# Optimization experiments

Hardware: AMD Instinct MI355X
Metric: run time of the kernel (lower is better)

Reference implementation:

```python
import jax, jax.numpy as jnp
import numpy as np

B, T, C, H, F = 4, 1024, 1024, 16, 4096
D = C // H

def _ln(x, g, b):
    m = x.mean(-1, keepdims=True)
    v = ((x - m) ** 2).mean(-1, keepdims=True)
    return (x - m) * jax.lax.rsqrt(v + 1e-5) * g + b

def setup_inputs() -> dict:
    key = jax.random.key(0)
    ks = jax.random.split(key, 9)
    p = lambda k, shape: jax.random.normal(k, shape, jnp.float32) * 0.02
    return dict(
        x=jax.random.normal(ks[0], (B, T, C), jnp.float32),
        context=jax.random.normal(ks[1], (B, T, C), jnp.float32),
        ln1_g=jnp.ones((C,), jnp.float32), ln1_b=jnp.zeros((C,), jnp.float32),
        qkv_w=p(ks[2], (C, 3 * C)), qkv_b=jnp.zeros((3 * C,), jnp.float32),
        attn_out_w=p(ks[3], (C, C)), attn_out_b=jnp.zeros((C,), jnp.float32),
        lnc_g=jnp.ones((C,), jnp.float32), lnc_b=jnp.zeros((C,), jnp.float32),
        q_w=p(ks[4], (C, C)), q_b=jnp.zeros((C,), jnp.float32),
        kv_w=p(ks[5], (C, 2 * C)), kv_b=jnp.zeros((2 * C,), jnp.float32),
        cross_out_w=p(ks[6], (C, C)), cross_out_b=jnp.zeros((C,), jnp.float32),
        ln2_g=jnp.ones((C,), jnp.float32), ln2_b=jnp.zeros((C,), jnp.float32),
        ffn_w1=p(ks[7], (C, F)), ffn_b1=jnp.zeros((F,), jnp.float32),
        ffn_w2=p(ks[8], (F, C)), ffn_b2=jnp.zeros((C,), jnp.float32),
    )

def reference(x, context, ln1_g, ln1_b, qkv_w, qkv_b, attn_out_w, attn_out_b,
              lnc_g, lnc_b, q_w, q_b, kv_w, kv_b, cross_out_w, cross_out_b,
              ln2_g, ln2_b, ffn_w1, ffn_b1, ffn_w2, ffn_b2):
    scale = 1.0 / np.sqrt(D)
    # --- causal self-attention ---
    h = _ln(x, ln1_g, ln1_b)
    qkv = (h @ qkv_w + qkv_b).reshape(B, T, 3, H, D)
    q, k, v = qkv[:, :, 0], qkv[:, :, 1], qkv[:, :, 2]  # [B,T,H,D]
    s = jnp.einsum('bqhd,bkhd->bhqk', q, k) * scale     # [B,H,T,T]
    causal = jnp.tril(jnp.ones((T, T), bool))
    s = jnp.where(causal, s, -jnp.inf)
    a = jax.nn.softmax(s, axis=-1)
    o = jnp.einsum('bhqk,bkhd->bqhd', a, v).reshape(B, T, C)
    x = x + o @ attn_out_w + attn_out_b
    # --- cross-attention (query=x, context=encoder) ---
    h = _ln(x, lnc_g, lnc_b)
    q = (h @ q_w + q_b).reshape(B, T, H, D)
    kv = (context @ kv_w + kv_b).reshape(B, T, 2, H, D)
    k, v = kv[:, :, 0], kv[:, :, 1]
    s = jnp.einsum('bqhd,bkhd->bhqk', q, k) * scale
    a = jax.nn.softmax(s, axis=-1)
    o = jnp.einsum('bhqk,bkhd->bqhd', a, v).reshape(B, T, C)
    x = x + o @ cross_out_w + cross_out_b
    # --- FFN (exact GELU as in torch default) ---
    h = _ln(x, ln2_g, ln2_b)
    h = jax.nn.gelu(h @ ffn_w1 + ffn_b1, approximate=False)
    return x + h @ ffn_w2 + ffn_b2
```

## Files before the change

### kernel.cpp

```cpp
#include <hip/hip_runtime.h>
#include <hip/hip_bf16.h>

#define BT 4096
#define TT 1024
#define HN 16

typedef __attribute__((ext_vector_type(8))) short bf16x8;
typedef __attribute__((ext_vector_type(4))) float f32x4;

__device__ __forceinline__ unsigned short f2bf(float f) {
    unsigned u = __builtin_bit_cast(unsigned, f);
    unsigned r = (u + 0x7fffu + ((u >> 16) & 1u)) >> 16;
    return (unsigned short)r;
}

__device__ __forceinline__ unsigned pk2bf(float a, float b) {
    return (unsigned)f2bf(a) | ((unsigned)f2bf(b) << 16);
}

__device__ __forceinline__ void g2l16(const void* g, void* l) {
    __builtin_amdgcn_global_load_lds(
        (__attribute__((address_space(1))) void*)(g),
        (__attribute__((address_space(3))) void*)(l), 16, 0, 0);
}

__device__ __forceinline__ float gelu_f(float v) {
    float t = v * (0.7978845608f + 0.0356774081f * v * v);
    float e = __expf(2.f * t);
    float th = 1.f - 2.f / (e + 1.f);
    return 0.5f * v * (1.f + th);
}

struct TransJobs {
    const float* W[7];
    unsigned short* Wt[7];
    int K[7], N[7];
    int start[8];
};

__global__ __launch_bounds__(256)
void transpose_all(TransJobs J)
{
    __shared__ float tile[32][33];
    int bx = blockIdx.x;
    int j = 0;
#pragma unroll
    for (int t = 0; t < 7; ++t)
        if (bx >= J.start[t + 1]) j = t + 1;
    int t = bx - J.start[j];
    int K = J.K[j], N = J.N[j];
    int ntx = N >> 5;
    int n0 = (t % ntx) * 32, k0 = (t / ntx) * 32;
    const float* W = J.W[j];
    unsigned short* Wt = J.Wt[j];
    int tx = threadIdx.x, ty = threadIdx.y;
#pragma unroll
    for (int i = ty; i < 32; i += 8)
        tile[i][tx] = W[(size_t)(k0 + i) * N + n0 + tx];
    __syncthreads();
#pragma unroll
    for (int i = ty; i < 32; i += 8)
        Wt[(size_t)(n0 + i) * K + k0 + tx] = f2bf(tile[tx][i]);
}

__global__ __launch_bounds__(256)
void transpose_v(const unsigned short* __restrict__ v, unsigned short* __restrict__ vt,
                 int stride)
{
    __shared__ unsigned short tile[32][33];
    int d0 = blockIdx.x * 32, t0 = blockIdx.y * 32, bh = blockIdx.z;
    int b = bh >> 4, h = bh & 15;
    int tx = threadIdx.x, ty = threadIdx.y;
#pragma unroll
    for (int i = ty; i < 32; i += 8)
        tile[i][tx] = v[((size_t)b * TT + t0 + i) * stride + h * 64 + d0 + tx];
    __syncthreads();
#pragma unroll
    for (int i = ty; i < 32; i += 8)
        vt[((size_t)bh * 64 + d0 + i) * TT + t0 + tx] = tile[tx][i];
}

__device__ __forceinline__
void ln_row(const float* __restrict__ xr, const float* __restrict__ g,
            const float* __restrict__ bta, unsigned short* __restrict__ outr,
            float* red)
{
    float4 v = ((const float4*)xr)[threadIdx.x];
    float s = v.x + v.y + v.z + v.w;
    float q = v.x*v.x + v.y*v.y + v.z*v.z + v.w*v.w;
#pragma unroll
    for (int m = 1; m < 64; m <<= 1) {
        s += __shfl_xor(s, m, 64);
        q += __shfl_xor(q, m, 64);
    }
    int wave = threadIdx.x >> 6;
    if ((threadIdx.x & 63) == 0) { red[wave] = s; red[4 + wave] = q; }
    __syncthreads();
    s = red[0] + red[1] + red[2] + red[3];
    q = red[4] + red[5] + red[6] + red[7];
    float mean = s * (1.f / 1024.f);
    float var  = q * (1.f / 1024.f) - mean * mean;
    float rstd = rsqrtf(var + 1e-5f);
    float4 gv = ((const float4*)g)[threadIdx.x];
    float4 bv = ((const float4*)bta)[threadIdx.x];
    uint2 o;
    o.x = pk2bf((v.x - mean) * rstd * gv.x + bv.x, (v.y - mean) * rstd * gv.y + bv.y);
    o.y = pk2bf((v.z - mean) * rstd * gv.z + bv.z, (v.w - mean) * rstd * gv.w + bv.w);
    ((uint2*)outr)[threadIdx.x] = o;
}

__global__ __launch_bounds__(256)
void ln_kernel(const float* __restrict__ x, const float* __restrict__ g,
               const float* __restrict__ bta, unsigned short* __restrict__ out)
{
    __shared__ float red[8];
    int row = blockIdx.x;
    ln_row(x + (size_t)row * 1024, g, bta, out + (size_t)row * 1024, red);
}

__global__ __launch_bounds__(256)
void ln_cast(const float* __restrict__ x, const float* __restrict__ g,
             const float* __restrict__ bta, unsigned short* __restrict__ outx,
             const float* __restrict__ ctx, unsigned short* __restrict__ outc)
{
    __shared__ float red[8];
    int bid = blockIdx.x;
    if (bid < BT) {
        ln_row(x + (size_t)bid * 1024, g, bta, outx + (size_t)bid * 1024, red);
    } else {
        size_t i = (size_t)(bid - BT) * 256 + threadIdx.x;
        float4 v = ((const float4*)ctx)[i];
        uint2 o;
        o.x = pk2bf(v.x, v.y);
        o.y = pk2bf(v.z, v.w);
        ((uint2*)outc)[i] = o;
    }
}

template<int MODE>
__device__ __forceinline__
void gemm_core(unsigned short* lA, unsigned short* lB,
               const unsigned short* __restrict__ A,
               const unsigned short* __restrict__ Bt,
               const float* __restrict__ bias,
               const float* __restrict__ res,
               void* __restrict__ outp,
               int N, int K, int m0, int n0, int kbeg, int kend)
{
    const int tid = threadIdx.x;
    const int wave = tid >> 6, lane = tid & 63;
    const int quad = lane >> 4, l16 = lane & 15;
    const int sw = l16 & 7;
    const int wN = (wave >> 1) * 64;
    const int wM = (wave & 1) * 64;

    f32x4 acc[4][4];
#pragma unroll
    for (int i = 0; i < 4; ++i)
#pragma unroll
        for (int j = 0; j < 4; ++j)
#pragma unroll
            for (int r = 0; r < 4; ++r) acc[i][j][r] = 0.f;

    for (int k0 = kbeg; k0 < kend; k0 += 64) {
        __syncthreads();
#pragma unroll
        for (int it = 0; it < 4; ++it) {
            int chunk = it * 256 + tid;
            int row = chunk >> 3, slot = chunk & 7;
            int kc = slot ^ (row & 7);
            g2l16(A  + (size_t)(m0 + row) * K + k0 + kc * 8, &lA[chunk * 8]);
            g2l16(Bt + (size_t)(n0 + row) * K + k0 + kc * 8, &lB[chunk * 8]);
        }
        __syncthreads();
#pragma unroll
        for (int kk = 0; kk < 64; kk += 32) {
            const int gc = (kk >> 3) + quad;
            const int sl = (gc ^ sw) * 8;
            bf16x8 af[4], bfr[4];
#pragma unroll
            for (int i = 0; i < 4; ++i)
                af[i] = *(const bf16x8*)&lB[(wN + i * 16 + l16) * 64 + sl];
#pragma unroll
            for (int j = 0; j < 4; ++j)
                bfr[j] = *(const bf16x8*)&lA[(wM + j * 16 + l16) * 64 + sl];
#pragma unroll
            for (int i = 0; i < 4; ++i)
#pragma unroll
                for (int j = 0; j < 4; ++j)
                    acc[i][j] = __builtin_amdgcn_mfma_f32_16x16x32_bf16(af[i], bfr[j], acc[i][j], 0, 0, 0);
        }
    }

#pragma unroll
    for (int i = 0; i < 4; ++i) {
        const int nb = n0 + wN + i * 16 + quad * 4;
        float4 bs;
        if (MODE != 3) bs = *(const float4*)&bias[nb];
#pragma unroll
        for (int j = 0; j < 4; ++j) {
            const int m = m0 + wM + j * 16 + l16;
            const size_t idx = (size_t)m * N + nb;
            float v0 = acc[i][j][0], v1 = acc[i][j][1];
            float v2 = acc[i][j][2], v3 = acc[i][j][3];
            if (MODE != 3) { v0 += bs.x; v1 += bs.y; v2 += bs.z; v3 += bs.w; }
            if (MODE == 1) { v0 = gelu_f(v0); v1 = gelu_f(v1); v2 = gelu_f(v2); v3 = gelu_f(v3); }
            if (MODE == 2) {
                float4 rr = *(const float4*)&res[idx];
                float4 o; o.x = v0 + rr.x; o.y = v1 + rr.y; o.z = v2 + rr.z; o.w = v3 + rr.w;
                *(float4*)((float*)outp + idx) = o;
            } else if (MODE == 3) {
                float4 o; o.x = v0; o.y = v1; o.z = v2; o.w = v3;
                *(float4*)((float*)outp + idx) = o;
            } else {
                uint2 u;
                u.x = pk2bf(v0, v1);
                u.y = pk2bf(v2, v3);
                *(uint2*)((unsigned short*)outp + idx) = u;
            }
        }
    }
}

template<int MODE>
__global__ __launch_bounds__(256)
void gemm_bt(const unsigned short* __restrict__ A,
             const unsigned short* __restrict__ Bt,
             const float* __restrict__ bias,
             const float* __restrict__ res,
             void* __restrict__ outp,
             int M, int N, int K)
{
    __shared__ unsigned short lA[128 * 64];
    __shared__ unsigned short lB[128 * 64];
    gemm_core<MODE>(lA, lB, A, Bt, bias, res, outp, N, K,
                    blockIdx.y * 128, blockIdx.x * 128, 0, K);
}

__global__ __launch_bounds__(256)
void gemm_dual(const unsigned short* __restrict__ A1, const unsigned short* __restrict__ B1,
               const float* __restrict__ b1, unsigned short* __restrict__ o1p, int N1, int nbx1,
               const unsigned short* __restrict__ A2, const unsigned short* __restrict__ B2,
               const float* __restrict__ b2, unsigned short* __restrict__ o2p, int N2,
               int K)
{
    __shared__ unsigned short lA[128 * 64];
    __shared__ unsigned short lB[128 * 64];
    int bx = blockIdx.x;
    if (bx < nbx1)
        gemm_core<0>(lA, lB, A1, B1, b1, nullptr, o1p, N1, K,
                     blockIdx.y * 128, bx * 128, 0, K);
    else
        gemm_core<0>(lA, lB, A2, B2, b2, nullptr, o2p, N2, K,
                     blockIdx.y * 128, (bx - nbx1) * 128, 0, K);
}

__global__ __launch_bounds__(256)
void gemm_splitk(const unsigned short* __restrict__ A,
                 const unsigned short* __restrict__ Bt,
                 float* __restrict__ part,
                 int M, int N, int K, int kslice)
{
    __shared__ unsigned short lA[128 * 64];
    __shared__ unsigned short lB[128 * 64];
    int kz = blockIdx.z;
    gemm_core<3>(lA, lB, A, Bt, nullptr, nullptr,
                 part + (size_t)kz * M * N, N, K,
                 blockIdx.y * 128, blockIdx.x * 128,
                 kz * kslice, (kz + 1) * kslice);
}

__global__ __launch_bounds__(256)
void reduce2(const float* __restrict__ part, const float* __restrict__ bias,
             const float* __restrict__ res, float* __restrict__ out, int MN)
{
    int i = blockIdx.x * 256 + threadIdx.x;
    const float4* p = (const float4*)part;
    int q = MN >> 2;
    float4 a = p[i], b = p[i + q];
    float4 bs = ((const float4*)bias)[i & 255];
    float4 rr = ((const float4*)res)[i];
    float4 o;
    o.x = a.x + b.x + bs.x + rr.x;
    o.y = a.y + b.y + bs.y + rr.y;
    o.z = a.z + b.z + bs.z + rr.z;
    o.w = a.w + b.w + bs.w + rr.w;
    ((float4*)out)[i] = o;
}

__global__ __launch_bounds__(256)
void gemm_small2(const unsigned short* __restrict__ A,
                 const unsigned short* __restrict__ Bt,
                 const float* __restrict__ bias,
                 const float* __restrict__ res,
                 float* __restrict__ outp,
                 int M, int N, int K)
{
    __shared__ unsigned short lA[64 * 64];
    __shared__ unsigned short lB[128 * 64];
    const int tid = threadIdx.x;
    const int wave = tid >> 6, lane = tid & 63;
    const int quad = lane >> 4, l16 = lane & 15;
    const int sw = l16 & 7;
    const int m0 = blockIdx.y * 64, n0 = blockIdx.x * 128;
    const int wM = (wave >> 1) * 32;
    const int wN = (wave & 1) * 64;

    f32x4 acc[4][2];
#pragma unroll
    for (int i = 0; i < 4; ++i)
#pragma unroll
        for (int j = 0; j < 2; ++j)
#pragma unroll
            for (int r = 0; r < 4; ++r) acc[i][j][r] = 0.f;

    for (int k0 = 0; k0 < K; k0 += 64) {
        __syncthreads();
#pragma unroll
        for (int it = 0; it < 6; ++it) {
            int chunk = it * 256 + tid;
            if (chunk < 512) {
                int row = chunk >> 3, slot = chunk & 7;
                int kc = slot ^ (row & 7);
                g2l16(A + (size_t)(m0 + row) * K + k0 + kc * 8, &lA[chunk * 8]);
            } else {
                int cb = chunk - 512;
                int row = cb >> 3, slot = cb & 7;
                int kc = slot ^ (row & 7);
                g2l16(Bt + (size_t)(n0 + row) * K + k0 + kc * 8, &lB[cb * 8]);
            }
        }
        __syncthreads();
#pragma unroll
        for (int kk = 0; kk < 64; kk += 32) {
            const int gc = (kk >> 3) + quad;
            const int sl = (gc ^ sw) * 8;
            bf16x8 af[4], bfr[2];
#pragma unroll
            for (int i = 0; i < 4; ++i)
                af[i] = *(const bf16x8*)&lB[(wN + i * 16 + l16) * 64 + sl];
#pragma unroll
            for (int j = 0; j < 2; ++j)
                bfr[j] = *(const bf16x8*)&lA[(wM + j * 16 + l16) * 64 + sl];
#pragma unroll
            for (int i = 0; i < 4; ++i)
#pragma unroll
                for (int j = 0; j < 2; ++j)
                    acc[i][j] = __builtin_amdgcn_mfma_f32_16x16x32_bf16(af[i], bfr[j], acc[i][j], 0, 0, 0);
        }
    }

#pragma unroll
    for (int i = 0; i < 4; ++i) {
        const int nb = n0 + wN + i * 16 + quad * 4;
        float4 bs = *(const float4*)&bias[nb];
#pragma unroll
        for (int j = 0; j < 2; ++j) {
            const int m = m0 + wM + j * 16 + l16;
            const size_t idx = (size_t)m * N + nb;
            float4 rr = *(const float4*)&res[idx];
            float4 o;
            o.x = acc[i][j][0] + bs.x + rr.x;
            o.y = acc[i][j][1] + bs.y + rr.y;
            o.z = acc[i][j][2] + bs.z + rr.z;
            o.w = acc[i][j][3] + bs.w + rr.w;
            *(float4*)&outp[idx] = o;
        }
    }
}

__global__ __launch_bounds__(256)
void attn_kernel(const unsigned short* __restrict__ qp,
                 const unsigned short* __restrict__ kp,
                 const unsigned short* __restrict__ vt,
                 unsigned short* __restrict__ op,
                 int qstride, int kstride, int causal)
{
    __shared__ unsigned short lK[64 * 72];
    __shared__ unsigned short lV[64 * 72];
    __shared__ unsigned short lP[4][16 * 72];

    const int tid = threadIdx.x;
    const int wave = tid >> 6, lane = tid & 63;
    const int quad = lane >> 4, l16 = lane & 15;
    const int bh = blockIdx.y, b = bh >> 4, h = bh & 15;
    const int qtile = causal ? (gridDim.x - 1 - blockIdx.x) : blockIdx.x;
    const int q0 = qtile * 64;
    const size_t rowbase = (size_t)b * TT;
    const int hoff = h * 64;
    const unsigned short* vbase = vt + (size_t)bh * 64 * TT;

    bf16x8 qf[2];
    {
        int qrow = q0 + wave * 16 + l16;
        const unsigned short* qrp = qp + (rowbase + qrow) * (size_t)qstride + hoff;
        qf[0] = *(const bf16x8*)(qrp + quad * 8);
        qf[1] = *(const bf16x8*)(qrp + 32 + quad * 8);
    }

    f32x4 oacc[4];
#pragma unroll
    for (int jd = 0; jd < 4; ++jd)
#pragma unroll
        for (int r = 0; r < 4; ++r) oacc[jd][r] = 0.f;
    float mrun = -1e30f, lrun = 0.f;

    const int nkt = causal ? (qtile + 1) : (TT / 64);
    for (int kt = 0; kt < nkt; ++kt) {
        __syncthreads();
#pragma unroll
        for (int it = 0; it < 2; ++it) {
            int c = it * 256 + tid;
            int r8 = c >> 3, cc = c & 7;
            *(bf16x8*)&lK[r8 * 72 + cc * 8] =
                *(const bf16x8*)(kp + (rowbase + kt * 64 + r8) * (size_t)kstride + hoff + cc * 8);
            *(bf16x8*)&lV[r8 * 72 + cc * 8] =
                *(const bf16x8*)(vbase + (size_t)r8 * TT + kt * 64 + cc * 8);
        }
        __syncthreads();

        f32x4 s[4];
#pragma unroll
        for (int i = 0; i < 4; ++i)
#pragma unroll
            for (int r = 0; r < 4; ++r) s[i][r] = 0.f;
#pragma unroll
        for (int kk = 0; kk < 2; ++kk) {
            bf16x8 kf[4];
#pragma unroll
            for (int i = 0; i < 4; ++i)
                kf[i] = *(const bf16x8*)&lK[(i * 16 + l16) * 72 + kk * 32 + quad * 8];
#pragma unroll
            for (int i = 0; i < 4; ++i)
                s[i] = __builtin_amdgcn_mfma_f32_16x16x32_bf16(kf[i], qf[kk], s[i], 0, 0, 0);
        }

        const int qg = q0 + wave * 16 + l16;
        const bool domask = (causal != 0) && (kt == qtile);
        float mloc = -1e30f;
#pragma unroll
        for (int i = 0; i < 4; ++i)
#pragma unroll
            for (int r = 0; r < 4; ++r) {
                float v = s[i][r] * 0.125f;
                if (domask) {
                    int kg = kt * 64 + i * 16 + quad * 4 + r;
                    if (kg > qg) v = -1e30f;
                }
                s[i][r] = v;
                mloc = fmaxf(mloc, v);
            }
        mloc = fmaxf(mloc, __shfl_xor(mloc, 16, 64));
        mloc = fmaxf(mloc, __shfl_xor(mloc, 32, 64));
        float mn = fmaxf(mrun, mloc);
        float alpha = __expf(mrun - mn);
        mrun = mn;
        float ls = 0.f;
#pragma unroll
        for (int i = 0; i < 4; ++i)
#pragma unroll
            for (int r = 0; r < 4; ++r) {
                float p = __expf(s[i][r] - mn);
                s[i][r] = p;
                ls += p;
            }
        ls += __shfl_xor(ls, 16, 64);
        ls += __shfl_xor(ls, 32, 64);
        lrun = lrun * alpha + ls;

        float arow[4];
#pragma unroll
        for (int r = 0; r < 4; ++r)
            arow[r] = __shfl(alpha, quad * 4 + r, 64);
#pragma unroll
        for (int jd = 0; jd < 4; ++jd)
#pragma unroll
            for (int r = 0; r < 4; ++r) oacc[jd][r] *= arow[r];

        unsigned short* pw = lP[wave];
#pragma unroll
        for (int i = 0; i < 4; ++i) {
            ushort4 pk;
            pk.x = f2bf(s[i][0]); pk.y = f2bf(s[i][1]);
            pk.z = f2bf(s[i][2]); pk.w = f2bf(s[i][3]);
            *(ushort4*)&pw[l16 * 72 + i * 16 + quad * 4] = pk;
        }

#pragma unroll
        for (int kk = 0; kk < 2; ++kk) {
            bf16x8 pf = *(const bf16x8*)&pw[l16 * 72 + kk * 32 + quad * 8];
            bf16x8 vf[4];
#pragma unroll
            for (int jd = 0; jd < 4; ++jd)
                vf[jd] = *(const bf16x8*)&lV[(jd * 16 + l16) * 72 + kk * 32 + quad * 8];
#pragma unroll
            for (int jd = 0; jd < 4; ++jd)
                oacc[jd] = __builtin_amdgcn_mfma_f32_16x16x32_bf16(pf, vf[jd], oacc[jd], 0, 0, 0);
        }
    }

    float ir[4];
#pragma unroll
    for (int r = 0; r < 4; ++r)
        ir[r] = 1.f / __shfl(lrun, quad * 4 + r, 64);
#pragma unroll
    for (int r = 0; r < 4; ++r) {
        int qg = q0 + wave * 16 + quad * 4 + r;
        unsigned short* orow = op + (rowbase + qg) * (size_t)1024 + hoff;
#pragma unroll
        for (int jd = 0; jd < 4; ++jd)
            orow[jd * 16 + l16] = f2bf(oacc[jd][r] * ir[r]);
    }
}

extern "C" void kernel_launch(void* const* d_in, const int* in_sizes, int n_in,
                              void* d_out, int out_size, void* d_ws, size_t ws_size,
                              hipStream_t stream)
{
    const float* x     = (const float*)d_in[0];
    const float* ctx   = (const float*)d_in[1];
    const float* ln1_g = (const float*)d_in[2];
    const float* ln1_b = (const float*)d_in[3];
    const float* qkv_w = (const float*)d_in[4];
    const float* qkv_b = (const float*)d_in[5];
    const float* aow   = (const float*)d_in[6];
    const float* aob   = (const float*)d_in[7];
    const float* lnc_g = (const float*)d_in[8];
    const float* lnc_b = (const float*)d_in[9];
    const float* q_w   = (const float*)d_in[10];
    const float* q_b   = (const float*)d_in[11];
    const float* kv_w  = (const float*)d_in[12];
    const float* kv_b  = (const float*)d_in[13];
    const float* cow   = (const float*)d_in[14];
    const float* cob   = (const float*)d_in[15];
    const float* ln2_g = (const float*)d_in[16];
    const float* ln2_b = (const float*)d_in[17];
    const float* f1w   = (const float*)d_in[18];
    const float* f1b   = (const float*)d_in[19];
    const float* f2w   = (const float*)d_in[20];
    const float* f2b   = (const float*)d_in[21];

    char* ws = (char*)d_ws;
    size_t off = 0;
    auto alloc = [&](size_t bytes) {
        char* p = ws + off;
        off += (bytes + 255) & ~(size_t)255;
        return p;
    };

    unsigned short* WtQKV = (unsigned short*)alloc((size_t)3072 * 1024 * 2);
    unsigned short* WtAO  = (unsigned short*)alloc((size_t)1024 * 1024 * 2);
    unsigned short* WtQ   = (unsigned short*)alloc((size_t)1024 * 1024 * 2);
    unsigned short* WtKV  = (unsigned short*)alloc((size_t)2048 * 1024 * 2);
    unsigned short* WtCO  = (unsigned short*)alloc((size_t)1024 * 1024 * 2);
    unsigned short* WtF1  = (unsigned short*)alloc((size_t)4096 * 1024 * 2);
    unsigned short* WtF2  = (unsigned short*)alloc((size_t)1024 * 4096 * 2);
    unsigned short* hA    = (unsigned short*)alloc((size_t)BT * 1024 * 2);
    unsigned short* ctxb  = (unsigned short*)alloc((size_t)BT * 1024 * 2);
    unsigned short* qkvb  = (unsigned short*)alloc((size_t)BT * 3072 * 2);
    unsigned short* o1    = (unsigned short*)alloc((size_t)BT * 1024 * 2);
    float*          x1    = (float*)alloc((size_t)BT * 1024 * 4);
    unsigned short* qb    = (unsigned short*)alloc((size_t)BT * 1024 * 2);
    unsigned short* kvb   = (unsigned short*)alloc((size_t)BT * 2048 * 2);
    unsigned short* o2    = (unsigned short*)alloc((size_t)BT * 1024 * 2);
    float*          x2    = (float*)alloc((size_t)BT * 1024 * 4);
    unsigned short* mid   = (unsigned short*)alloc((size_t)BT * 4096 * 2);
    unsigned short* vT1   = (unsigned short*)alloc((size_t)BT * 1024 * 2);
    unsigned short* vT2   = (unsigned short*)alloc((size_t)BT * 1024 * 2);

    float* partials = (float*)qkvb;

    TransJobs J;
    J.W[0]=qkv_w; J.Wt[0]=WtQKV; J.K[0]=1024; J.N[0]=3072;
    J.W[1]=aow;   J.Wt[1]=WtAO;  J.K[1]=1024; J.N[1]=1024;
    J.W[2]=q_w;   J.Wt[2]=WtQ;   J.K[2]=1024; J.N[2]=1024;
    J.W[3]=kv_w;  J.Wt[3]=WtKV;  J.K[3]=1024; J.N[3]=2048;
    J.W[4]=cow;   J.Wt[4]=WtCO;  J.K[4]=1024; J.N[4]=1024;
    J.W[5]=f1w;   J.Wt[5]=WtF1;  J.K[5]=1024; J.N[5]=4096;
    J.W[6]=f2w;   J.Wt[6]=WtF2;  J.K[6]=4096; J.N[6]=1024;
    int acc = 0;
    for (int j = 0; j < 7; ++j) {
        J.start[j] = acc;
        acc += (J.N[j] / 32) * (J.K[j] / 32);
    }
    J.start[7] = acc;

    dim3 tb(32, 8);
    transpose_all<<<acc, tb, 0, stream>>>(J);

    ln_cast<<<2 * BT, 256, 0, stream>>>(x, ln1_g, ln1_b, hA, ctx, ctxb);
    gemm_bt<0><<<dim3(3072/128, BT/128), 256, 0, stream>>>(hA, WtQKV, qkv_b, nullptr, qkvb, BT, 3072, 1024);
    transpose_v<<<dim3(2, TT/32, 64), tb, 0, stream>>>(qkvb + 2048, vT1, 3072);
    attn_kernel<<<dim3(TT/64, 64), 256, 0, stream>>>(qkvb, qkvb + 1024, vT1, o1, 3072, 3072, 1);
    gemm_small2<<<dim3(1024/128, BT/64), 256, 0, stream>>>(o1, WtAO, aob, x, x1, BT, 1024, 1024);

    ln_kernel<<<BT, 256, 0, stream>>>(x1, lnc_g, lnc_b, hA);
    gemm_dual<<<dim3(1024/128 + 2048/128, BT/128), 256, 0, stream>>>(
        hA, WtQ, q_b, qb, 1024, 1024/128,
        ctxb, WtKV, kv_b, kvb, 2048, 1024);
    transpose_v<<<dim3(2, TT/32, 64), tb, 0, stream>>>(kvb + 1024, vT2, 2048);
    attn_kernel<<<dim3(TT/64, 64), 256, 0, stream>>>(qb, kvb, vT2, o2, 1024, 2048, 0);
    gemm_small2<<<dim3(1024/128, BT/64), 256, 0, stream>>>(o2, WtCO, cob, x1, x2, BT, 1024, 1024);

    ln_kernel<<<BT, 256, 0, stream>>>(x2, ln2_g, ln2_b, hA);
    gemm_bt<1><<<dim3(4096/128, BT/128), 256, 0, stream>>>(hA, WtF1, f1b, nullptr, mid, BT, 4096, 1024);
    gemm_splitk<<<dim3(1024/128, BT/128, 2), 256, 0, stream>>>(mid, WtF2, partials, BT, 1024, 4096, 2048);
    reduce2<<<BT * 1024 / 4 / 256, 256, 0, stream>>>(partials, f2b, x2, (float*)d_out, BT * 1024);
}
```

Baseline: 538.3 us.

## Switch GEMMs to 32x32x16 MFMA and merge weight prep into one kernel

The GEMM cores now use the 32x32x16 bf16 MFMA with f32x16 accumulators in place of 16x16x32 tiles. This cuts the number of LDS fragment reads per output and the instruction count. The weight transpose kernel is also merged with the LN/context-cast kernel into a single prep launch, removing one launch and the serial dependency between them. The epilogue indexing is rewritten for the 32x32 output layout, which risks mistakes in the layout mapping and raises register pressure.

```diff
diff --git a/kernel.cpp b/kernel.cpp
--- a/kernel.cpp
+++ b/kernel.cpp
@@ -7,6 +7,7 @@
 
 typedef __attribute__((ext_vector_type(8))) short bf16x8;
 typedef __attribute__((ext_vector_type(4))) float f32x4;
+typedef __attribute__((ext_vector_type(16))) float f32x16;
 
 __device__ __forceinline__ unsigned short f2bf(float f) {
     unsigned u = __builtin_bit_cast(unsigned, f);
@@ -37,48 +38,6 @@
     int K[7], N[7];
     int start[8];
 };
-
-__global__ __launch_bounds__(256)
-void transpose_all(TransJobs J)
-{
-    __shared__ float tile[32][33];
-    int bx = blockIdx.x;
-    int j = 0;
-#pragma unroll
-    for (int t = 0; t < 7; ++t)
-        if (bx >= J.start[t + 1]) j = t + 1;
-    int t = bx - J.start[j];
-    int K = J.K[j], N = J.N[j];
-    int ntx = N >> 5;
-    int n0 = (t % ntx) * 32, k0 = (t / ntx) * 32;
-    const float* W = J.W[j];
-    unsigned short* Wt = J.Wt[j];
-    int tx = threadIdx.x, ty = threadIdx.y;
-#pragma unroll
-    for (int i = ty; i < 32; i += 8)
-        tile[i][tx] = W[(size_t)(k0 + i) * N + n0 + tx];
-    __syncthreads();
-#pragma unroll
-    for (int i = ty; i < 32; i += 8)
-        Wt[(size_t)(n0 + i) * K + k0 + tx] = f2bf(tile[tx][i]);
-}
-
-__global__ __launch_bounds__(256)
-void transpose_v(const unsigned short* __restrict__ v, unsigned short* __restrict__ vt,
-                 int stride)
-{
-    __shared__ unsigned short tile[32][33];
-    int d0 = blockIdx.x * 32, t0 = blockIdx.y * 32, bh = blockIdx.z;
-    int b = bh >> 4, h = bh & 15;
-    int tx = threadIdx.x, ty = threadIdx.y;
-#pragma unroll
-    for (int i = ty; i < 32; i += 8)
-        tile[i][tx] = v[((size_t)b * TT + t0 + i) * stride + h * 64 + d0 + tx];
-    __syncthreads();
-#pragma unroll
-    for (int i = ty; i < 32; i += 8)
-        vt[((size_t)bh * 64 + d0 + i) * TT + t0 + tx] = tile[tx][i];
-}
 
 __device__ __forceinline__
 void ln_row(const float* __restrict__ xr, const float* __restrict__ g,
@@ -110,31 +69,71 @@
 }
 
 __global__ __launch_bounds__(256)
-void ln_kernel(const float* __restrict__ x, const float* __restrict__ g,
-               const float* __restrict__ bta, unsigned short* __restrict__ out)
-{
-    __shared__ float red[8];
-    int row = blockIdx.x;
-    ln_row(x + (size_t)row * 1024, g, bta, out + (size_t)row * 1024, red);
-}
-
-__global__ __launch_bounds__(256)
-void ln_cast(const float* __restrict__ x, const float* __restrict__ g,
-             const float* __restrict__ bta, unsigned short* __restrict__ outx,
-             const float* __restrict__ ctx, unsigned short* __restrict__ outc)
-{
+void prep_kernel(TransJobs J, const float* __restrict__ x,
+                 const float* __restrict__ g, const float* __restrict__ bta,
+                 unsigned short* __restrict__ outx,
+                 const float* __restrict__ ctx, unsigned short* __restrict__ outc)
+{
+    __shared__ float tile[32][33];
     __shared__ float red[8];
     int bid = blockIdx.x;
-    if (bid < BT) {
-        ln_row(x + (size_t)bid * 1024, g, bta, outx + (size_t)bid * 1024, red);
+    const int nT = J.start[7];
+    if (bid < nT) {
+        int j = 0;
+#pragma unroll
+        for (int t = 0; t < 7; ++t)
+            if (bid >= J.start[t + 1]) j = t + 1;
+        int t = bid - J.start[j];
+        int K = J.K[j], N = J.N[j];
+        int ntx = N >> 5;
+        int n0 = (t % ntx) * 32, k0 = (t / ntx) * 32;
+        const float* W = J.W[j];
+        unsigned short* Wt = J.Wt[j];
+        int tx = threadIdx.x & 31, ty = threadIdx.x >> 5;
+#pragma unroll
+        for (int i = ty; i < 32; i += 8)
+            tile[i][tx] = W[(size_t)(k0 + i) * N + n0 + tx];
+        __syncthreads();
+#pragma unroll
+        for (int i = ty; i < 32; i += 8)
+            Wt[(size_t)(n0 + i) * K + k0 + tx] = f2bf(tile[tx][i]);
+    } else if (bid < nT + BT) {
+        int row = bid - nT;
+        ln_row(x + (size_t)row * 1024, g, bta, outx + (size_t)row * 1024, red);
     } else {
-        size_t i = (size_t)(bid - BT) * 256 + threadIdx.x;
+        size_t i = (size_t)(bid - nT - BT) * 256 + threadIdx.x;
         float4 v = ((const float4*)ctx)[i];
         uint2 o;
         o.x = pk2bf(v.x, v.y);
         o.y = pk2bf(v.z, v.w);
         ((uint2*)outc)[i] = o;
     }
+}
+
+__global__ __launch_bounds__(256)
+void ln_kernel(const float* __restrict__ x, const float* __restrict__ g,
+               const float* __restrict__ bta, unsigned short* __restrict__ out)
+{
+    __shared__ float red[8];
+    int row = blockIdx.x;
+    ln_row(x + (size_t)row * 1024, g, bta, out + (size_t)row * 1024, red);
+}
+
+__global__ __launch_bounds__(256)
+void transpose_v(const unsigned short* __restrict__ v, unsigned short* __restrict__ vt,
+                 int stride)
+{
+    __shared__ unsigned short tile[32][33];
+    int d0 = blockIdx.x * 32, t0 = blockIdx.y * 32, bh = blockIdx.z;
+    int b = bh >> 4, h = bh & 15;
+    int tx = threadIdx.x, ty = threadIdx.y;
+#pragma unroll
+    for (int i = ty; i < 32; i += 8)
+        tile[i][tx] = v[((size_t)b * TT + t0 + i) * stride + h * 64 + d0 + tx];
+    __syncthreads();
+#pragma unroll
+    for (int i = ty; i < 32; i += 8)
+        vt[((size_t)bh * 64 + d0 + i) * TT + t0 + tx] = tile[tx][i];
 }
 
 template<int MODE>
@@ -149,18 +148,18 @@
 {
     const int tid = threadIdx.x;
     const int wave = tid >> 6, lane = tid & 63;
-    const int quad = lane >> 4, l16 = lane & 15;
-    const int sw = l16 & 7;
+    const int l32 = lane & 31, half = lane >> 5;
+    const int sw = l32 & 7;
     const int wN = (wave >> 1) * 64;
     const int wM = (wave & 1) * 64;
 
-    f32x4 acc[4][4];
-#pragma unroll
-    for (int i = 0; i < 4; ++i)
-#pragma unroll
-        for (int j = 0; j < 4; ++j)
-#pragma unroll
-            for (int r = 0; r < 4; ++r) acc[i][j][r] = 0.f;
+    f32x16 acc[2][2];
+#pragma unroll
+    for (int i = 0; i < 2; ++i)
+#pragma unroll
+        for (int j = 0; j < 2; ++j)
+#pragma unroll
+            for (int r = 0; r < 16; ++r) acc[i][j][r] = 0.f;
 
     for (int k0 = kbeg; k0 < kend; k0 += 64) {
         __syncthreads();
@@ -174,49 +173,52 @@
         }
         __syncthreads();
 #pragma unroll
-        for (int kk = 0; kk < 64; kk += 32) {
-            const int gc = (kk >> 3) + quad;
+        for (int ks = 0; ks < 4; ++ks) {
+            const int gc = ks * 2 + half;
             const int sl = (gc ^ sw) * 8;
-            bf16x8 af[4], bfr[4];
-#pragma unroll
-            for (int i = 0; i < 4; ++i)
-                af[i] = *(const bf16x8*)&lB[(wN + i * 16 + l16) * 64 + sl];
-#pragma unroll
-            for (int j = 0; j < 4; ++j)
-                bfr[j] = *(const bf16x8*)&lA[(wM + j * 16 + l16) * 64 + sl];
-#pragma unroll
-            for (int i = 0; i < 4; ++i)
-#pragma unroll
-                for (int j = 0; j < 4; ++j)
-                    acc[i][j] = __builtin_amdgcn_mfma_f32_16x16x32_bf16(af[i], bfr[j], acc[i][j], 0, 0, 0);
-        }
-    }
-
-#pragma unroll
-    for (int i = 0; i < 4; ++i) {
-        const int nb = n0 + wN + i * 16 + quad * 4;
-        float4 bs;
-        if (MODE != 3) bs = *(const float4*)&bias[nb];
-#pragma unroll
-        for (int j = 0; j < 4; ++j) {
-            const int m = m0 + wM + j * 16 + l16;
-            const size_t idx = (size_t)m * N + nb;
-            float v0 = acc[i][j][0], v1 = acc[i][j][1];
-            float v2 = acc[i][j][2], v3 = acc[i][j][3];
-            if (MODE != 3) { v0 += bs.x; v1 += bs.y; v2 += bs.z; v3 += bs.w; }
-            if (MODE == 1) { v0 = gelu_f(v0); v1 = gelu_f(v1); v2 = gelu_f(v2); v3 = gelu_f(v3); }
-            if (MODE == 2) {
-                float4 rr = *(const float4*)&res[idx];
-                float4 o; o.x = v0 + rr.x; o.y = v1 + rr.y; o.z = v2 + rr.z; o.w = v3 + rr.w;
-                *(float4*)((float*)outp + idx) = o;
-            } else if (MODE == 3) {
-                float4 o; o.x = v0; o.y = v1; o.z = v2; o.w = v3;
-                *(float4*)((float*)outp + idx) = o;
-            } else {
-                uint2 u;
-                u.x = pk2bf(v0, v1);
-                u.y = pk2bf(v2, v3);
-                *(uint2*)((unsigned short*)outp + idx) = u;
+            bf16x8 af[2], bfr[2];
+#pragma unroll
+            for (int i = 0; i < 2; ++i)
+                af[i] = *(const bf16x8*)&lB[(wN + i * 32 + l32) * 64 + sl];
+#pragma unroll
+            for (int j = 0; j < 2; ++j)
+                bfr[j] = *(const bf16x8*)&lA[(wM + j * 32 + l32) * 64 + sl];
+#pragma unroll
+            for (int i = 0; i < 2; ++i)
+#pragma unroll
+                for (int j = 0; j < 2; ++j)
+                    acc[i][j] = __builtin_amdgcn_mfma_f32_32x32x16_bf16(af[i], bfr[j], acc[i][j], 0, 0, 0);
+        }
+    }
+
+#pragma unroll
+    for (int i = 0; i < 2; ++i) {
+#pragma unroll
+        for (int g = 0; g < 4; ++g) {
+            const int nb = n0 + wN + i * 32 + g * 8 + half * 4;
+            float4 bs;
+            if (MODE != 3) bs = *(const float4*)&bias[nb];
+#pragma unroll
+            for (int j = 0; j < 2; ++j) {
+                const int m = m0 + wM + j * 32 + l32;
+                const size_t idx = (size_t)m * N + nb;
+                float v0 = acc[i][j][g * 4 + 0], v1 = acc[i][j][g * 4 + 1];
+                float v2 = acc[i][j][g * 4 + 2], v3 = acc[i][j][g * 4 + 3];
+                if (MODE != 3) { v0 += bs.x; v1 += bs.y; v2 += bs.z; v3 += bs.w; }
+                if (MODE == 1) { v0 = gelu_f(v0); v1 = gelu_f(v1); v2 = gelu_f(v2); v3 = gelu_f(v3); }
+                if (MODE == 2) {
+                    float4 rr = *(const float4*)&res[idx];
+                    float4 o; o.x = v0 + rr.x; o.y = v1 + rr.y; o.z = v2 + rr.z; o.w = v3 + rr.w;
+                    *(float4*)((float*)outp + idx) = o;
+                } else if (MODE == 3) {
+                    float4 o; o.x = v0; o.y = v1; o.z = v2; o.w = v3;
+                    *(float4*)((float*)outp + idx) = o;
+                } else {
+                    uint2 u;
+                    u.x = pk2bf(v0, v1);
+                    u.y = pk2bf(v2, v3);
+                    *(uint2*)((unsigned short*)outp + idx) = u;
+                }
             }
         }
     }
@@ -300,19 +302,17 @@
     __shared__ unsigned short lB[128 * 64];
     const int tid = threadIdx.x;
     const int wave = tid >> 6, lane = tid & 63;
-    const int quad = lane >> 4, l16 = lane & 15;
-    const int sw = l16 & 7;
+    const int l32 = lane & 31, half = lane >> 5;
+    const int sw = l32 & 7;
     const int m0 = blockIdx.y * 64, n0 = blockIdx.x * 128;
     const int wM = (wave >> 1) * 32;
     const int wN = (wave & 1) * 64;
 
-    f32x4 acc[4][2];
-#pragma unroll
-    for (int i = 0; i < 4; ++i)
-#pragma unroll
-        for (int j = 0; j < 2; ++j)
-#pragma unroll
-            for (int r = 0; r < 4; ++r) acc[i][j][r] = 0.f;
+    f32x16 acc[2];
+#pragma unroll
+    for (int i = 0; i < 2; ++i)
+#pragma unroll
+        for (int r = 0; r < 16; ++r) acc[i][r] = 0.f;
 
     for (int k0 = 0; k0 < K; k0 += 64) {
         __syncthreads();
@@ -332,38 +332,34 @@
         }
         __syncthreads();
 #pragma unroll
-        for (int kk = 0; kk < 64; kk += 32) {
-            const int gc = (kk >> 3) + quad;
+        for (int ks = 0; ks < 4; ++ks) {
+            const int gc = ks * 2 + half;
             const int sl = (gc ^ sw) * 8;
-            bf16x8 af[4], bfr[2];
-#pragma unroll
-            for (int i = 0; i < 4; ++i)
-                af[i] = *(const bf16x8*)&lB[(wN + i * 16 + l16) * 64 + sl];
-#pragma unroll
-            for (int j = 0; j < 2; ++j)
-                bfr[j] = *(const bf16x8*)&lA[(wM + j * 16 + l16) * 64 + sl];
-#pragma unroll
-            for (int i = 0; i < 4; ++i)
-#pragma unroll
-                for (int j = 0; j < 2; ++j)
-                    acc[i][j] = __builtin_amdgcn_mfma_f32_16x16x32_bf16(af[i], bfr[j], acc[i][j], 0, 0, 0);
-        }
-    }
-
-#pragma unroll
-    for (int i = 0; i < 4; ++i) {
-        const int nb = n0 + wN + i * 16 + quad * 4;
-        float4 bs = *(const float4*)&bias[nb];
-#pragma unroll
-        for (int j = 0; j < 2; ++j) {
-            const int m = m0 + wM + j * 16 + l16;
+            bf16x8 bfr = *(const bf16x8*)&lA[(wM + l32) * 64 + sl];
+            bf16x8 af[2];
+#pragma unroll
+            for (int i = 0; i < 2; ++i)
+                af[i] = *(const bf16x8*)&lB[(wN + i * 32 + l32) * 64 + sl];
+#pragma unroll
+            for (int i = 0; i < 2; ++i)
+                acc[i] = __builtin_amdgcn_mfma_f32_32x32x16_bf16(af[i], bfr, acc[i], 0, 0, 0);
+        }
+    }
+
+#pragma unroll
+    for (int i = 0; i < 2; ++i) {
+#pragma unroll
+        for (int g = 0; g < 4; ++g) {
+            const int nb = n0 + wN + i * 32 + g * 8 + half * 4;
+            float4 bs = *(const float4*)&bias[nb];
+            const int m = m0 + wM + l32;
             const size_t idx = (size_t)m * N + nb;
             float4 rr = *(const float4*)&res[idx];
             float4 o;
-            o.x = acc[i][j][0] + bs.x + rr.x;
-            o.y = acc[i][j][1] + bs.y + rr.y;
-            o.z = acc[i][j][2] + bs.z + rr.z;
-            o.w = acc[i][j][3] + bs.w + rr.w;
+            o.x = acc[i][g * 4 + 0] + bs.x + rr.x;
+            o.y = acc[i][g * 4 + 1] + bs.y + rr.y;
+            o.z = acc[i][g * 4 + 2] + bs.z + rr.z;
+            o.w = acc[i][g * 4 + 3] + bs.w + rr.w;
             *(float4*)&outp[idx] = o;
         }
     }
@@ -586,9 +582,9 @@
     J.start[7] = acc;
 
     dim3 tb(32, 8);
-    transpose_all<<<acc, tb, 0, stream>>>(J);
-
-    ln_cast<<<2 * BT, 256, 0, stream>>>(x, ln1_g, ln1_b, hA, ctx, ctxb);
+
+    prep_kernel<<<acc + 2 * BT, 256, 0, stream>>>(J, x, ln1_g, ln1_b, hA, ctx, ctxb);
+
     gemm_bt<0><<<dim3(3072/128, BT/128), 256, 0, stream>>>(hA, WtQKV, qkv_b, nullptr, qkvb, BT, 3072, 1024);
     transpose_v<<<dim3(2, TT/32, 64), tb, 0, stream>>>(qkvb + 2048, vT1, 3072);
     attn_kernel<<<dim3(TT/64, 64), 256, 0, stream>>>(qkvb, qkvb + 1024, vT1, o1, 3072, 3072, 1);
```

Result: no change. 533.2 us (-1.0%).
